# Optimization experiments

Measured on AMD Instinct MI355X. Metric: run time of the kernel, lower is better.

Reference implementation:

```python
import jax, jax.numpy as jnp
import numpy as np

B, S, D, H = 2, 2048, 1024, 16
DK = D // H
MAX_REL = 2047          # clip range for relative distances
REL_DIM = 64            # rel_embedding dim, summed over


def setup_inputs() -> dict:
    key = jax.random.key(0)
    ks = jax.random.split(key, 12)
    sc = 1.0 / np.sqrt(D)
    inp = {
        "q": jax.random.normal(ks[0], (B, S, D), jnp.float32),
        "k": jax.random.normal(ks[1], (B, S, D), jnp.float32),
        "v": jax.random.normal(ks[2], (B, S, D), jnp.float32),
        "Wq": jax.random.normal(ks[3], (D, D), jnp.float32) * sc,
        "bq": jnp.zeros((D,), jnp.float32),
        "Wk": jax.random.normal(ks[4], (D, D), jnp.float32) * sc,
        "bk": jnp.zeros((D,), jnp.float32),
        "Wv": jax.random.normal(ks[5], (D, D), jnp.float32) * sc,
        "bv": jnp.zeros((D,), jnp.float32),
        "Wo": jax.random.normal(ks[6], (D, D), jnp.float32) * sc,
        "bo": jnp.zeros((D,), jnp.float32),
        "rel_table": jax.random.normal(ks[7], (2 * MAX_REL + 1, REL_DIM), jnp.float32) * 0.02,
        "mask": jnp.tril(jnp.ones((1, 1, S, S), jnp.bool_)),  # causal
    }
    return inp


def reference(q, k, v, Wq, bq, Wk, bk, Wv, bv, Wo, bo, rel_table, mask):
    def split_heads(x):
        # [B,S,D] -> [B,H,S,DK]
        return x.reshape(B, -1, H, DK).transpose(0, 2, 1, 3)

    Q = split_heads(q @ Wq + bq)
    K = split_heads(k @ Wk + bk)
    V = split_heads(v @ Wv + bv)

    scores = jnp.einsum("bhqd,bhkd->bhqk", Q, K) / jnp.sqrt(jnp.float32(DK))

    # relative position bias: table[clip(j - i)] summed over rel dim -> [S,S]
    rel_idx = jnp.clip(jnp.arange(S)[None, :] - jnp.arange(S)[:, None],
                       -MAX_REL, MAX_REL) + MAX_REL
    rel_bias = rel_table[rel_idx].sum(-1)  # [S,S]
    scores = scores + rel_bias[None, None]

    scores = jnp.where(mask, scores, jnp.float32(-1e20))
    attn = jax.nn.softmax(scores, axis=-1)

    out = jnp.einsum("bhqk,bhkd->bhqd", attn, V)
    out = out.transpose(0, 2, 1, 3).reshape(B, -1, D)
    return out @ Wo + bo
```

## Files before the change

kernel.cpp:

```cpp
#include <hip/hip_runtime.h>

#define SEQ 2048
#define DIM 1024
#define NH 16
#define HD 64
#define NB 2

typedef __bf16 bf16x8 __attribute__((ext_vector_type(8)));
typedef float f32x4 __attribute__((ext_vector_type(4)));
typedef float f32x4v __attribute__((ext_vector_type(4)));
typedef float f32x4u __attribute__((ext_vector_type(4), aligned(4)));
typedef unsigned short us8 __attribute__((ext_vector_type(8)));
typedef unsigned short us4 __attribute__((ext_vector_type(4)));

#define LOG2E 1.44269504f

__device__ __forceinline__ unsigned short bfbits(float f) {
  __bf16 h = (__bf16)f;
  return __builtin_bit_cast(unsigned short, h);
}

__global__ __launch_bounds__(256) void wconv4_kernel(
    const float* __restrict__ W0, const float* __restrict__ W1,
    const float* __restrict__ W2, const float* __restrict__ W3,
    unsigned short* __restrict__ Wt, const float* __restrict__ rel_table,
    float* __restrict__ relsum, const float* __restrict__ Aq,
    const float* __restrict__ Ak, const float* __restrict__ Av,
    unsigned short* __restrict__ Bq, unsigned short* __restrict__ Bk,
    unsigned short* __restrict__ Bv) {
  int z = blockIdx.z;
  int tid = threadIdx.x;
  if (z == 4) {
    int ti = blockIdx.y * 16 + blockIdx.x;
    int i = ti * 256 + tid;
    if (i < 4095) {
      const f32x4v* row = reinterpret_cast<const f32x4v*>(rel_table + (size_t)i * 64);
      float s = 0.f;
      for (int d = 0; d < 16; ++d) {
        f32x4v v = row[d];
        s += v[0] + v[1] + v[2] + v[3];
      }
      relsum[i] = s * LOG2E;
    }
    return;
  }
  if (z >= 5) {
    const float* src = (z == 5) ? Aq : (z == 6) ? Ak : Av;
    unsigned short* dst = (z == 5) ? Bq : (z == 6) ? Bk : Bv;
    int bid2 = blockIdx.y * 16 + blockIdx.x;
    int c0 = bid2 * 256 + tid;
    for (int j = 0; j < 8; ++j) {
      size_t e = ((size_t)(c0 + j * 65536)) * 8;
      f32x4v v0 = *reinterpret_cast<const f32x4v*>(src + e);
      f32x4v v1 = *reinterpret_cast<const f32x4v*>(src + e + 4);
      us8 o;
      o[0] = bfbits(v0[0]); o[1] = bfbits(v0[1]); o[2] = bfbits(v0[2]); o[3] = bfbits(v0[3]);
      o[4] = bfbits(v1[0]); o[5] = bfbits(v1[1]); o[6] = bfbits(v1[2]); o[7] = bfbits(v1[3]);
      *reinterpret_cast<us8*>(dst + e) = o;
    }
    return;
  }
  __shared__ unsigned short T[64][68];
  const float* W = (z == 0) ? W0 : (z == 1) ? W1 : (z == 2) ? W2 : W3;
  unsigned short* out = Wt + (size_t)z * 1024 * 1024;
  int r0 = blockIdx.y * 64;
  int c0 = blockIdx.x * 64;
  for (int it = 0; it < 4; ++it) {
    int s = tid + it * 256;
    int r = s >> 4;
    int c4 = (s & 15) * 4;
    f32x4v v = *reinterpret_cast<const f32x4v*>(W + (size_t)(r0 + r) * 1024 + c0 + c4);
    us4 o;
    o[0] = bfbits(v[0]); o[1] = bfbits(v[1]); o[2] = bfbits(v[2]); o[3] = bfbits(v[3]);
    *reinterpret_cast<us4*>(&T[r][c4]) = o;
  }
  __syncthreads();
  for (int it = 0; it < 2; ++it) {
    int s = tid + it * 256;
    int n = s >> 3;
    int k8 = (s & 7) * 8;
    us8 o;
    for (int e = 0; e < 8; ++e) o[e] = T[k8 + e][n];
    *reinterpret_cast<us8*>(out + (size_t)(c0 + n) * 1024 + r0 + k8) = o;
  }
}

__global__ __launch_bounds__(256) void gemm_qkv_kernel(
    const unsigned short* __restrict__ Aq, const unsigned short* __restrict__ Ak,
    const unsigned short* __restrict__ Av, const unsigned short* __restrict__ WTb,
    const float* __restrict__ bq, const float* __restrict__ bk,
    const float* __restrict__ bv, unsigned short* __restrict__ Qb,
    unsigned short* __restrict__ Kb, unsigned short* __restrict__ Vt,
    float qscale) {
  constexpr int N = 1024, K = 1024;
  int o = (blockIdx.x & 7) * 192 + (blockIdx.x >> 3);
  int z = o >> 9;
  int r2 = o & 511;
  int row0 = (r2 >> 4) * 128;
  int col0 = (r2 & 15) * 64;
  const unsigned short* A = (z == 0) ? Aq : (z == 1) ? Ak : Av;
  const unsigned short* WT = WTb + (size_t)z * N * K;
  const float* bias = (z == 0) ? bq : (z == 1) ? bk : bv;
  float oscale = (z == 0) ? qscale : 1.0f;

  int tid = threadIdx.x;
  int w = tid >> 6;
  int lane = tid & 63;
  int lg = lane >> 4;
  int li = lane & 15;
  int wr = (w >> 1) * 64;
  int wc = (w & 1) * 32;

  __shared__ unsigned short As[2][128][72];
  __shared__ unsigned short Ws[2][64][72];

  us8 ab16[4];
  us8 wreg[2];

#define GLOAD(KS)                                                         \
  {                                                                       \
    int k0 = (KS) * 64;                                                   \
    for (int it = 0; it < 4; ++it) {                                      \
      int s = tid + it * 256;                                             \
      int r = s >> 3;                                                     \
      int cg = (s & 7) * 8;                                               \
      ab16[it] = *reinterpret_cast<const us8*>(                           \
          A + (size_t)(row0 + r) * K + k0 + cg);                          \
    }                                                                     \
    for (int it = 0; it < 2; ++it) {                                      \
      int s = tid + it * 256;                                             \
      int c = s >> 3;                                                     \
      int kg = (s & 7) * 8;                                               \
      wreg[it] = *reinterpret_cast<const us8*>(                           \
          WT + (size_t)(col0 + c) * K + k0 + kg);                         \
    }                                                                     \
  }

#define SWRITE(B)                                                         \
  {                                                                       \
    for (int it = 0; it < 4; ++it) {                                      \
      int s = tid + it * 256;                                             \
      int r = s >> 3;                                                     \
      int cg = (s & 7) * 8;                                               \
      *reinterpret_cast<us8*>(&As[B][r][cg]) = ab16[it];                  \
    }                                                                     \
    for (int it = 0; it < 2; ++it) {                                      \
      int s = tid + it * 256;                                             \
      int c = s >> 3;                                                     \
      int kg = (s & 7) * 8;                                               \
      *reinterpret_cast<us8*>(&Ws[B][c][kg]) = wreg[it];                  \
    }                                                                     \
  }

  f32x4 acc[4][2] = {};

  GLOAD(0);
  SWRITE(0);
  GLOAD(1);
  __syncthreads();

  for (int ks = 0; ks < 16; ++ks) {
    if (ks < 15) SWRITE((ks + 1) & 1);
    if (ks < 14) GLOAD(ks + 2);
    int B = ks & 1;
    for (int kk = 0; kk < 2; ++kk) {
      bf16x8 af[4], bfr[2];
      for (int m = 0; m < 4; ++m)
        af[m] = *reinterpret_cast<const bf16x8*>(&As[B][wr + m * 16 + li][kk * 32 + lg * 8]);
      for (int n = 0; n < 2; ++n)
        bfr[n] = *reinterpret_cast<const bf16x8*>(&Ws[B][wc + n * 16 + li][kk * 32 + lg * 8]);
      for (int m = 0; m < 4; ++m)
        for (int n = 0; n < 2; ++n)
          acc[m][n] = __builtin_amdgcn_mfma_f32_16x16x32_bf16(af[m], bfr[n], acc[m][n], 0, 0, 0);
    }
    __syncthreads();
  }

  for (int m = 0; m < 4; ++m)
    for (int n = 0; n < 2; ++n) {
      int row = row0 + wr + m * 16 + lg * 4;
      int col = col0 + wc + n * 16 + li;
      float v4[4];
      for (int r = 0; r < 4; ++r) v4[r] = (acc[m][n][r] + bias[col]) * oscale;
      if (z == 2) {
        int bb = row >> 11, seq = row & 2047;
        int hh = col >> 6, dk = col & 63;
        us4 o4;
        o4[0] = bfbits(v4[0]); o4[1] = bfbits(v4[1]);
        o4[2] = bfbits(v4[2]); o4[3] = bfbits(v4[3]);
        *reinterpret_cast<us4*>(
            Vt + ((size_t)(bb * NH + hh) * HD + dk) * SEQ + seq) = o4;
      } else {
        unsigned short* Cp = (z == 0) ? Qb : Kb;
        for (int r = 0; r < 4; ++r)
          Cp[(size_t)(row + r) * N + col] = bfbits(v4[r]);
      }
    }
#undef GLOAD
#undef SWRITE
}

__global__ __launch_bounds__(256) void gemm_out_kernel(
    const unsigned short* __restrict__ A, const unsigned short* __restrict__ WT,
    const float* __restrict__ bias, float* __restrict__ Cp) {
  constexpr int N = 1024, K = 1024;
  int o = ((blockIdx.x & 7) << 6) | (blockIdx.x >> 3);
  int col0 = (o & 15) * 64;
  int row0 = (o >> 4) * 128;
  int tid = threadIdx.x;
  int w = tid >> 6;
  int lane = tid & 63;
  int lg = lane >> 4;
  int li = lane & 15;
  int wr = (w >> 1) * 64;
  int wc = (w & 1) * 32;

  __shared__ unsigned short As[2][128][72];
  __shared__ unsigned short Ws[2][64][72];

  us8 ab16[4];
  us8 wreg[2];

#define GLOAD(KS)                                                         \
  {                                                                       \
    int k0 = (KS) * 64;                                                   \
    for (int it = 0; it < 4; ++it) {                                      \
      int s = tid + it * 256;                                             \
      int r = s >> 3;                                                     \
      int cg = (s & 7) * 8;                                               \
      ab16[it] = *reinterpret_cast<const us8*>(                           \
          A + (size_t)(row0 + r) * K + k0 + cg);                          \
    }                                                                     \
    for (int it = 0; it < 2; ++it) {                                      \
      int s = tid + it * 256;                                             \
      int c = s >> 3;                                                     \
      int kg = (s & 7) * 8;                                               \
      wreg[it] = *reinterpret_cast<const us8*>(                           \
          WT + (size_t)(col0 + c) * K + k0 + kg);                         \
    }                                                                     \
  }

#define SWRITE(B)                                                         \
  {                                                                       \
    for (int it = 0; it < 4; ++it) {                                      \
      int s = tid + it * 256;                                             \
      int r = s >> 3;                                                     \
      int cg = (s & 7) * 8;                                               \
      *reinterpret_cast<us8*>(&As[B][r][cg]) = ab16[it];                  \
    }                                                                     \
    for (int it = 0; it < 2; ++it) {                                      \
      int s = tid + it * 256;                                             \
      int c = s >> 3;                                                     \
      int kg = (s & 7) * 8;                                               \
      *reinterpret_cast<us8*>(&Ws[B][c][kg]) = wreg[it];                  \
    }                                                                     \
  }

  f32x4 acc[4][2] = {};

  GLOAD(0);
  SWRITE(0);
  GLOAD(1);
  __syncthreads();

  for (int ks = 0; ks < 16; ++ks) {
    if (ks < 15) SWRITE((ks + 1) & 1);
    if (ks < 14) GLOAD(ks + 2);
    int B = ks & 1;
    for (int kk = 0; kk < 2; ++kk) {
      bf16x8 af[4], bfr[2];
      for (int m = 0; m < 4; ++m)
        af[m] = *reinterpret_cast<const bf16x8*>(&As[B][wr + m * 16 + li][kk * 32 + lg * 8]);
      for (int n = 0; n < 2; ++n)
        bfr[n] = *reinterpret_cast<const bf16x8*>(&Ws[B][wc + n * 16 + li][kk * 32 + lg * 8]);
      for (int m = 0; m < 4; ++m)
        for (int n = 0; n < 2; ++n)
          acc[m][n] = __builtin_amdgcn_mfma_f32_16x16x32_bf16(af[m], bfr[n], acc[m][n], 0, 0, 0);
    }
    __syncthreads();
  }

  for (int m = 0; m < 4; ++m)
    for (int n = 0; n < 2; ++n)
      for (int r = 0; r < 4; ++r) {
        int row = row0 + wr + m * 16 + lg * 4 + r;
        int col = col0 + wc + n * 16 + li;
        Cp[(size_t)row * N + col] = acc[m][n][r] + bias[col];
      }
#undef GLOAD
#undef SWRITE
}

__global__ __launch_bounds__(256) void attn_kernel(
    const unsigned short* __restrict__ Qb, const unsigned short* __restrict__ Kb,
    const unsigned short* __restrict__ Vt, const float* __restrict__ relsum,
    unsigned short* __restrict__ Ob) {
  int o = ((blockIdx.x & 7) << 6) | (blockIdx.x >> 3);
  int p = o & 15;
  int h = (o >> 4) & 15;
  int b = o >> 8;

  int tid = threadIdx.x;
  int w = tid >> 6;
  int lane = tid & 63;
  int lg = lane >> 4;
  int li = lane & 15;

  __shared__ unsigned short Ks[128][72];
  __shared__ unsigned short VtF[2][64 * 72];
  __shared__ __bf16 Ps[4][16][136];
  __shared__ float rel_lds[2176];

  for (int it = 0; it < 3; ++it) {
    int slot = tid + it * 256;
    if (slot < 544)
      *reinterpret_cast<f32x4v*>(&rel_lds[slot * 4]) =
          *reinterpret_cast<const f32x4v*>(&relsum[slot * 4]);
  }

  int key0 = tid >> 3;
  int cg0 = (tid & 7) * 8;
  int dk0 = tid >> 3;
  int k8 = (tid & 7) * 8;
  const unsigned short* kptr = Kb + ((size_t)(b * SEQ + key0)) * DIM + h * HD + cg0;
  const unsigned short* vtp = Vt + ((size_t)(b * NH + h) * HD + dk0) * SEQ + k8;

  unsigned vidx0 = ((unsigned)(dk0 * 72 + k8)) ^ ((((unsigned)dk0 >> 3) & 7u) << 3);
  unsigned vidx1 = ((unsigned)((dk0 + 32) * 72 + k8)) ^
                   ((((unsigned)(dk0 + 32) >> 3) & 7u) << 3);

  us8 krg[4], vrg[4];

#define LOAD_REGS(TT)                                                     \
  {                                                                       \
    size_t koff = (size_t)(TT) * 128 * DIM;                               \
    krg[0] = *reinterpret_cast<const us8*>(kptr + koff);                  \
    krg[1] = *reinterpret_cast<const us8*>(kptr + koff + 32 * DIM);       \
    krg[2] = *reinterpret_cast<const us8*>(kptr + koff + 64 * DIM);       \
    krg[3] = *reinterpret_cast<const us8*>(kptr + koff + 96 * DIM);       \
    vrg[0] = *reinterpret_cast<const us8*>(vtp + (TT) * 128);             \
    vrg[1] = *reinterpret_cast<const us8*>(vtp + 32 * SEQ + (TT) * 128);  \
    vrg[2] = *reinterpret_cast<const us8*>(vtp + (TT) * 128 + 64);        \
    vrg[3] = *reinterpret_cast<const us8*>(vtp + 32 * SEQ + (TT) * 128 + 64); \
  }

#define WRITE_TILE()                                                     \
  {                                                                      \
    *reinterpret_cast<us8*>(&Ks[key0][cg0]) = krg[0];                    \
    *reinterpret_cast<us8*>(&Ks[key0 + 32][cg0]) = krg[1];               \
    *reinterpret_cast<us8*>(&Ks[key0 + 64][cg0]) = krg[2];               \
    *reinterpret_cast<us8*>(&Ks[key0 + 96][cg0]) = krg[3];               \
    *reinterpret_cast<us8*>(&VtF[0][vidx0]) = vrg[0];                    \
    *reinterpret_cast<us8*>(&VtF[0][vidx1]) = vrg[1];                    \
    *reinterpret_cast<us8*>(&VtF[1][vidx0]) = vrg[2];                    \
    *reinterpret_cast<us8*>(&VtF[1][vidx1]) = vrg[3];                    \
  }

  LOAD_REGS(0);

  for (int ph = 0; ph < 2; ++ph) {
    int qt = ph ? p : (31 - p);
    int nkv = (qt + 2) >> 1;

    int qrow = qt * 64 + w * 16 + li;
    const unsigned short* qb = Qb + ((size_t)(b * SEQ + qrow)) * DIM + h * HD;
    bf16x8 qa0 = *reinterpret_cast<const bf16x8*>(qb + lg * 8);
    bf16x8 qa1 = *reinterpret_cast<const bf16x8*>(qb + 32 + lg * 8);

    f32x4 o_acc[4] = {};
    float m_row[4], l_row[4];
    for (int r = 0; r < 4; ++r) { m_row[r] = -3e38f; l_row[r] = 0.f; }
    int i0 = qt * 64 + w * 16 + lg * 4;

    for (int t = 0; t < nkv; ++t) {
      __syncthreads();
      WRITE_TILE();
      __syncthreads();

      if (!(ph == 1 && t == nkv - 1)) {
        int nextT = (t + 1 < nkv) ? (t + 1) : 0;
        LOAD_REGS(nextT);
      }

      f32x4 s_acc[8] = {};
      __builtin_amdgcn_s_setprio(1);
      for (int kk = 0; kk < 2; ++kk) {
        bf16x8 qa = kk ? qa1 : qa0;
        for (int n = 0; n < 8; ++n) {
          bf16x8 kb = *reinterpret_cast<const bf16x8*>(&Ks[n * 16 + li][kk * 32 + lg * 8]);
          s_acc[n] = __builtin_amdgcn_mfma_f32_16x16x32_bf16(qa, kb, s_acc[n], 0, 0, 0);
        }
      }
      __builtin_amdgcn_s_setprio(0);

      float tmax[4] = {-3e38f, -3e38f, -3e38f, -3e38f};
      int Cbase = t * 128 - (qt * 64 + w * 16 + lg * 4) + li + 2047;
      if (t == nkv - 1) {
        for (int n = 0; n < 8; ++n) {
          int Cn = Cbase + n * 16;
          f32x4u rel4 = *reinterpret_cast<const f32x4u*>(&rel_lds[Cn - 3]);
          for (int r = 0; r < 4; ++r) {
            float sv = s_acc[n][r] + rel4[3 - r];
            sv = (Cn - r > 2047) ? -1e30f : sv;
            s_acc[n][r] = sv;
            tmax[r] = fmaxf(tmax[r], sv);
          }
        }
      } else {
        for (int n = 0; n < 8; ++n) {
          int Cn = Cbase + n * 16;
          f32x4u rel4 = *reinterpret_cast<const f32x4u*>(&rel_lds[Cn - 3]);
          for (int r = 0; r < 4; ++r) {
            float sv = s_acc[n][r] + rel4[3 - r];
            s_acc[n][r] = sv;
            tmax[r] = fmaxf(tmax[r], sv);
          }
        }
      }

      bool okl = true;
      for (int r = 0; r < 4; ++r) okl &= (tmax[r] <= m_row[r] + 8.f);
      if (!__all(okl)) {
        for (int msk = 1; msk < 16; msk <<= 1)
          for (int r = 0; r < 4; ++r)
            tmax[r] = fmaxf(tmax[r], __shfl_xor(tmax[r], msk));
        for (int r = 0; r < 4; ++r) {
          float mn = fmaxf(m_row[r], tmax[r]);
          float al = exp2f(m_row[r] - mn);
          m_row[r] = mn;
          l_row[r] *= al;
          o_acc[0][r] *= al; o_acc[1][r] *= al;
          o_acc[2][r] *= al; o_acc[3][r] *= al;
        }
      }

      for (int n = 0; n < 8; ++n)
        for (int r = 0; r < 4; ++r) {
          float e = exp2f(s_acc[n][r] - m_row[r]);
          s_acc[n][r] = e;
          l_row[r] += e;
        }

      for (int n = 0; n < 8; ++n)
        for (int r = 0; r < 4; ++r)
          Ps[w][lg * 4 + r][n * 16 + li] = (__bf16)s_acc[n][r];
      asm volatile("s_waitcnt lgkmcnt(0)" ::: "memory");
      __builtin_amdgcn_sched_barrier(0);

      __builtin_amdgcn_s_setprio(1);
      for (int kstep = 0; kstep < 4; ++kstep) {
        int half = kstep >> 1;
        int kk = kstep & 1;
        bf16x8 pa = *reinterpret_cast<const bf16x8*>(&Ps[w][li][kstep * 32 + lg * 8]);
        for (int n = 0; n < 4; ++n) {
          int dk = n * 16 + li;
          unsigned idx = ((unsigned)(dk * 72 + kk * 32 + lg * 8)) ^
                         ((((unsigned)dk >> 3) & 7u) << 3);
          bf16x8 vb = *reinterpret_cast<const bf16x8*>(&VtF[half][idx]);
          o_acc[n] = __builtin_amdgcn_mfma_f32_16x16x32_bf16(pa, vb, o_acc[n], 0, 0, 0);
        }
      }
      __builtin_amdgcn_s_setprio(0);
    }

    for (int msk = 1; msk < 16; msk <<= 1)
      for (int r = 0; r < 4; ++r) l_row[r] += __shfl_xor(l_row[r], msk);
    float inv_l[4];
    for (int r = 0; r < 4; ++r) inv_l[r] = 1.f / l_row[r];
    for (int n = 0; n < 4; ++n)
      for (int r = 0; r < 4; ++r) {
        int row = i0 + r;
        int dk = n * 16 + li;
        Ob[((size_t)(b * SEQ + row)) * DIM + h * HD + dk] =
            bfbits(o_acc[n][r] * inv_l[r]);
      }
  }
#undef LOAD_REGS
#undef WRITE_TILE
}

extern "C" void kernel_launch(void* const* d_in, const int* in_sizes, int n_in,
                              void* d_out, int out_size, void* d_ws, size_t ws_size,
                              hipStream_t stream) {
  const float* q = (const float*)d_in[0];
  const float* k = (const float*)d_in[1];
  const float* v = (const float*)d_in[2];
  const float* Wq = (const float*)d_in[3];
  const float* bq = (const float*)d_in[4];
  const float* Wk = (const float*)d_in[5];
  const float* bk = (const float*)d_in[6];
  const float* Wv = (const float*)d_in[7];
  const float* bv = (const float*)d_in[8];
  const float* Wo = (const float*)d_in[9];
  const float* bo = (const float*)d_in[10];
  const float* rel = (const float*)d_in[11];

  char* ws = (char*)d_ws;
  const size_t MATB = (size_t)NB * SEQ * DIM * sizeof(unsigned short);
  const size_t WTE = (size_t)DIM * DIM;
  unsigned short* Qb = (unsigned short*)(ws);
  unsigned short* Kb = (unsigned short*)(ws + MATB);
  unsigned short* Vt = (unsigned short*)(ws + 2 * MATB);
  unsigned short* Ob = (unsigned short*)(ws + 3 * MATB);
  float* relsum = (float*)(ws + 4 * MATB);
  unsigned short* WT = (unsigned short*)(ws + 4 * MATB + 65536);

  unsigned short* Abq = (unsigned short*)d_out;
  unsigned short* Abk = (unsigned short*)d_out + (size_t)NB * SEQ * DIM;
  unsigned short* Abv = Ob;

  wconv4_kernel<<<dim3(16, 16, 8), 256, 0, stream>>>(
      Wq, Wk, Wv, Wo, WT, rel, relsum, q, k, v, Abq, Abk, Abv);

  const float qscale = 0.125f * LOG2E;
  gemm_qkv_kernel<<<dim3(1536), 256, 0, stream>>>(Abq, Abk, Abv, WT, bq, bk, bv,
                                                  Qb, Kb, Vt, qscale);

  attn_kernel<<<dim3(512), 256, 0, stream>>>(Qb, Kb, Vt, relsum, Ob);

  gemm_out_kernel<<<dim3(512), 256, 0, stream>>>(Ob, WT + 3 * WTE, bo, (float*)d_out);
}
```

Baseline: 136.9 us.

## Split paired causal query tiles into one block each with 64-key tiles

The attention kernel no longer pairs a long and a short query tile in one block for load balance. It now launches one block per (batch, head, query tile), 1024 blocks in total, ordered longest-first and grouped by XCD. KV tiles shrink from 128 to 64 keys, so the causal diagonal tile wastes less masked work and LDS and register use drop, which may allow higher occupancy. In exchange each block does less work per barrier, K/V loads are repeated across more blocks, and load balance relies on the hardware scheduler rather than explicit pairing.

```diff
diff --git a/kernel.cpp b/kernel.cpp
--- a/kernel.cpp
+++ b/kernel.cpp
@@ -295,10 +295,12 @@
     const unsigned short* __restrict__ Qb, const unsigned short* __restrict__ Kb,
     const unsigned short* __restrict__ Vt, const float* __restrict__ relsum,
     unsigned short* __restrict__ Ob) {
-  int o = ((blockIdx.x & 7) << 6) | (blockIdx.x >> 3);
-  int p = o & 15;
-  int h = (o >> 4) & 15;
-  int b = o >> 8;
+  int r0_ = blockIdx.x >> 3;
+  int xcd = blockIdx.x & 7;
+  int qt = 31 - (r0_ >> 2);
+  int bh = xcd * 4 + (r0_ & 3);
+  int h = bh & 15;
+  int b = bh >> 4;
 
   int tid = threadIdx.x;
   int w = tid >> 6;
@@ -306,14 +308,14 @@
   int lg = lane >> 4;
   int li = lane & 15;
 
-  __shared__ unsigned short Ks[128][72];
-  __shared__ unsigned short VtF[2][64 * 72];
-  __shared__ __bf16 Ps[4][16][136];
-  __shared__ float rel_lds[2176];
+  __shared__ unsigned short Ks[64][72];
+  __shared__ unsigned short VtF[64 * 72];
+  __shared__ __bf16 Ps[4][16][72];
+  __shared__ float rel_lds[2112];
 
   for (int it = 0; it < 3; ++it) {
     int slot = tid + it * 256;
-    if (slot < 544)
+    if (slot < 528)
       *reinterpret_cast<f32x4v*>(&rel_lds[slot * 4]) =
           *reinterpret_cast<const f32x4v*>(&relsum[slot * 4]);
   }
@@ -329,152 +331,134 @@
   unsigned vidx1 = ((unsigned)((dk0 + 32) * 72 + k8)) ^
                    ((((unsigned)(dk0 + 32) >> 3) & 7u) << 3);
 
-  us8 krg[4], vrg[4];
+  us8 krg0, krg1, vrg0, vrg1;
 
 #define LOAD_REGS(TT)                                                     \
   {                                                                       \
-    size_t koff = (size_t)(TT) * 128 * DIM;                               \
-    krg[0] = *reinterpret_cast<const us8*>(kptr + koff);                  \
-    krg[1] = *reinterpret_cast<const us8*>(kptr + koff + 32 * DIM);       \
-    krg[2] = *reinterpret_cast<const us8*>(kptr + koff + 64 * DIM);       \
-    krg[3] = *reinterpret_cast<const us8*>(kptr + koff + 96 * DIM);       \
-    vrg[0] = *reinterpret_cast<const us8*>(vtp + (TT) * 128);             \
-    vrg[1] = *reinterpret_cast<const us8*>(vtp + 32 * SEQ + (TT) * 128);  \
-    vrg[2] = *reinterpret_cast<const us8*>(vtp + (TT) * 128 + 64);        \
-    vrg[3] = *reinterpret_cast<const us8*>(vtp + 32 * SEQ + (TT) * 128 + 64); \
-  }
-
-#define WRITE_TILE()                                                     \
-  {                                                                      \
-    *reinterpret_cast<us8*>(&Ks[key0][cg0]) = krg[0];                    \
-    *reinterpret_cast<us8*>(&Ks[key0 + 32][cg0]) = krg[1];               \
-    *reinterpret_cast<us8*>(&Ks[key0 + 64][cg0]) = krg[2];               \
-    *reinterpret_cast<us8*>(&Ks[key0 + 96][cg0]) = krg[3];               \
-    *reinterpret_cast<us8*>(&VtF[0][vidx0]) = vrg[0];                    \
-    *reinterpret_cast<us8*>(&VtF[0][vidx1]) = vrg[1];                    \
-    *reinterpret_cast<us8*>(&VtF[1][vidx0]) = vrg[2];                    \
-    *reinterpret_cast<us8*>(&VtF[1][vidx1]) = vrg[3];                    \
+    size_t koff = (size_t)(TT) * 64 * DIM;                                \
+    krg0 = *reinterpret_cast<const us8*>(kptr + koff);                    \
+    krg1 = *reinterpret_cast<const us8*>(kptr + koff + 32 * DIM);         \
+    vrg0 = *reinterpret_cast<const us8*>(vtp + (TT) * 64);                \
+    vrg1 = *reinterpret_cast<const us8*>(vtp + 32 * SEQ + (TT) * 64);     \
+  }
+
+#define WRITE_TILE()                                                      \
+  {                                                                       \
+    *reinterpret_cast<us8*>(&Ks[key0][cg0]) = krg0;                       \
+    *reinterpret_cast<us8*>(&Ks[key0 + 32][cg0]) = krg1;                  \
+    *reinterpret_cast<us8*>(&VtF[vidx0]) = vrg0;                          \
+    *reinterpret_cast<us8*>(&VtF[vidx1]) = vrg1;                          \
   }
 
   LOAD_REGS(0);
 
-  for (int ph = 0; ph < 2; ++ph) {
-    int qt = ph ? p : (31 - p);
-    int nkv = (qt + 2) >> 1;
-
-    int qrow = qt * 64 + w * 16 + li;
-    const unsigned short* qb = Qb + ((size_t)(b * SEQ + qrow)) * DIM + h * HD;
-    bf16x8 qa0 = *reinterpret_cast<const bf16x8*>(qb + lg * 8);
-    bf16x8 qa1 = *reinterpret_cast<const bf16x8*>(qb + 32 + lg * 8);
-
-    f32x4 o_acc[4] = {};
-    float m_row[4], l_row[4];
-    for (int r = 0; r < 4; ++r) { m_row[r] = -3e38f; l_row[r] = 0.f; }
-    int i0 = qt * 64 + w * 16 + lg * 4;
-
-    for (int t = 0; t < nkv; ++t) {
-      __syncthreads();
-      WRITE_TILE();
-      __syncthreads();
-
-      if (!(ph == 1 && t == nkv - 1)) {
-        int nextT = (t + 1 < nkv) ? (t + 1) : 0;
-        LOAD_REGS(nextT);
-      }
-
-      f32x4 s_acc[8] = {};
-      __builtin_amdgcn_s_setprio(1);
-      for (int kk = 0; kk < 2; ++kk) {
-        bf16x8 qa = kk ? qa1 : qa0;
-        for (int n = 0; n < 8; ++n) {
-          bf16x8 kb = *reinterpret_cast<const bf16x8*>(&Ks[n * 16 + li][kk * 32 + lg * 8]);
-          s_acc[n] = __builtin_amdgcn_mfma_f32_16x16x32_bf16(qa, kb, s_acc[n], 0, 0, 0);
+  int qrow = qt * 64 + w * 16 + li;
+  const unsigned short* qb = Qb + ((size_t)(b * SEQ + qrow)) * DIM + h * HD;
+  bf16x8 qa0 = *reinterpret_cast<const bf16x8*>(qb + lg * 8);
+  bf16x8 qa1 = *reinterpret_cast<const bf16x8*>(qb + 32 + lg * 8);
+
+  f32x4 o_acc[4] = {};
+  float m_row[4], l_row[4];
+  for (int r = 0; r < 4; ++r) { m_row[r] = -3e38f; l_row[r] = 0.f; }
+  int i0 = qt * 64 + w * 16 + lg * 4;
+
+  for (int t = 0; t <= qt; ++t) {
+    __syncthreads();
+    WRITE_TILE();
+    __syncthreads();
+
+    if (t < qt) LOAD_REGS(t + 1);
+
+    f32x4 s_acc[4] = {};
+    __builtin_amdgcn_s_setprio(1);
+    for (int kk = 0; kk < 2; ++kk) {
+      bf16x8 qa = kk ? qa1 : qa0;
+      for (int n = 0; n < 4; ++n) {
+        bf16x8 kb = *reinterpret_cast<const bf16x8*>(&Ks[n * 16 + li][kk * 32 + lg * 8]);
+        s_acc[n] = __builtin_amdgcn_mfma_f32_16x16x32_bf16(qa, kb, s_acc[n], 0, 0, 0);
+      }
+    }
+    __builtin_amdgcn_s_setprio(0);
+
+    float tmax[4] = {-3e38f, -3e38f, -3e38f, -3e38f};
+    int Cbase = (t - qt) * 64 - (w * 16 + lg * 4) + li + 2047;
+    if (t == qt) {
+      for (int n = 0; n < 4; ++n) {
+        int Cn = Cbase + n * 16;
+        f32x4u rel4 = *reinterpret_cast<const f32x4u*>(&rel_lds[Cn - 3]);
+        for (int r = 0; r < 4; ++r) {
+          float sv = s_acc[n][r] + rel4[3 - r];
+          sv = (Cn - r > 2047) ? -1e30f : sv;
+          s_acc[n][r] = sv;
+          tmax[r] = fmaxf(tmax[r], sv);
         }
       }
-      __builtin_amdgcn_s_setprio(0);
-
-      float tmax[4] = {-3e38f, -3e38f, -3e38f, -3e38f};
-      int Cbase = t * 128 - (qt * 64 + w * 16 + lg * 4) + li + 2047;
-      if (t == nkv - 1) {
-        for (int n = 0; n < 8; ++n) {
-          int Cn = Cbase + n * 16;
-          f32x4u rel4 = *reinterpret_cast<const f32x4u*>(&rel_lds[Cn - 3]);
-          for (int r = 0; r < 4; ++r) {
-            float sv = s_acc[n][r] + rel4[3 - r];
-            sv = (Cn - r > 2047) ? -1e30f : sv;
-            s_acc[n][r] = sv;
-            tmax[r] = fmaxf(tmax[r], sv);
-          }
+    } else {
+      for (int n = 0; n < 4; ++n) {
+        int Cn = Cbase + n * 16;
+        f32x4u rel4 = *reinterpret_cast<const f32x4u*>(&rel_lds[Cn - 3]);
+        for (int r = 0; r < 4; ++r) {
+          float sv = s_acc[n][r] + rel4[3 - r];
+          s_acc[n][r] = sv;
+          tmax[r] = fmaxf(tmax[r], sv);
         }
-      } else {
-        for (int n = 0; n < 8; ++n) {
-          int Cn = Cbase + n * 16;
-          f32x4u rel4 = *reinterpret_cast<const f32x4u*>(&rel_lds[Cn - 3]);
-          for (int r = 0; r < 4; ++r) {
-            float sv = s_acc[n][r] + rel4[3 - r];
-            s_acc[n][r] = sv;
-            tmax[r] = fmaxf(tmax[r], sv);
-          }
-        }
-      }
-
-      bool okl = true;
-      for (int r = 0; r < 4; ++r) okl &= (tmax[r] <= m_row[r] + 8.f);
-      if (!__all(okl)) {
-        for (int msk = 1; msk < 16; msk <<= 1)
-          for (int r = 0; r < 4; ++r)
-            tmax[r] = fmaxf(tmax[r], __shfl_xor(tmax[r], msk));
-        for (int r = 0; r < 4; ++r) {
-          float mn = fmaxf(m_row[r], tmax[r]);
-          float al = exp2f(m_row[r] - mn);
-          m_row[r] = mn;
-          l_row[r] *= al;
-          o_acc[0][r] *= al; o_acc[1][r] *= al;
-          o_acc[2][r] *= al; o_acc[3][r] *= al;
-        }
-      }
-
-      for (int n = 0; n < 8; ++n)
-        for (int r = 0; r < 4; ++r) {
-          float e = exp2f(s_acc[n][r] - m_row[r]);
-          s_acc[n][r] = e;
-          l_row[r] += e;
-        }
-
-      for (int n = 0; n < 8; ++n)
+      }
+    }
+
+    bool okl = true;
+    for (int r = 0; r < 4; ++r) okl &= (tmax[r] <= m_row[r] + 8.f);
+    if (!__all(okl)) {
+      for (int msk = 1; msk < 16; msk <<= 1)
         for (int r = 0; r < 4; ++r)
-          Ps[w][lg * 4 + r][n * 16 + li] = (__bf16)s_acc[n][r];
-      asm volatile("s_waitcnt lgkmcnt(0)" ::: "memory");
-      __builtin_amdgcn_sched_barrier(0);
-
-      __builtin_amdgcn_s_setprio(1);
-      for (int kstep = 0; kstep < 4; ++kstep) {
-        int half = kstep >> 1;
-        int kk = kstep & 1;
-        bf16x8 pa = *reinterpret_cast<const bf16x8*>(&Ps[w][li][kstep * 32 + lg * 8]);
-        for (int n = 0; n < 4; ++n) {
-          int dk = n * 16 + li;
-          unsigned idx = ((unsigned)(dk * 72 + kk * 32 + lg * 8)) ^
-                         ((((unsigned)dk >> 3) & 7u) << 3);
-          bf16x8 vb = *reinterpret_cast<const bf16x8*>(&VtF[half][idx]);
-          o_acc[n] = __builtin_amdgcn_mfma_f32_16x16x32_bf16(pa, vb, o_acc[n], 0, 0, 0);
-        }
-      }
-      __builtin_amdgcn_s_setprio(0);
-    }
-
-    for (int msk = 1; msk < 16; msk <<= 1)
-      for (int r = 0; r < 4; ++r) l_row[r] += __shfl_xor(l_row[r], msk);
-    float inv_l[4];
-    for (int r = 0; r < 4; ++r) inv_l[r] = 1.f / l_row[r];
+          tmax[r] = fmaxf(tmax[r], __shfl_xor(tmax[r], msk));
+      for (int r = 0; r < 4; ++r) {
+        float mn = fmaxf(m_row[r], tmax[r]);
+        float al = exp2f(m_row[r] - mn);
+        m_row[r] = mn;
+        l_row[r] *= al;
+        o_acc[0][r] *= al; o_acc[1][r] *= al;
+        o_acc[2][r] *= al; o_acc[3][r] *= al;
+      }
+    }
+
     for (int n = 0; n < 4; ++n)
       for (int r = 0; r < 4; ++r) {
-        int row = i0 + r;
+        float e = exp2f(s_acc[n][r] - m_row[r]);
+        s_acc[n][r] = e;
+        l_row[r] += e;
+      }
+
+    for (int n = 0; n < 4; ++n)
+      for (int r = 0; r < 4; ++r)
+        Ps[w][lg * 4 + r][n * 16 + li] = (__bf16)s_acc[n][r];
+    asm volatile("s_waitcnt lgkmcnt(0)" ::: "memory");
+    __builtin_amdgcn_sched_barrier(0);
+
+    __builtin_amdgcn_s_setprio(1);
+    for (int kk = 0; kk < 2; ++kk) {
+      bf16x8 pa = *reinterpret_cast<const bf16x8*>(&Ps[w][li][kk * 32 + lg * 8]);
+      for (int n = 0; n < 4; ++n) {
         int dk = n * 16 + li;
-        Ob[((size_t)(b * SEQ + row)) * DIM + h * HD + dk] =
-            bfbits(o_acc[n][r] * inv_l[r]);
-      }
-  }
+        unsigned idx = ((unsigned)(dk * 72 + kk * 32 + lg * 8)) ^
+                       ((((unsigned)dk >> 3) & 7u) << 3);
+        bf16x8 vb = *reinterpret_cast<const bf16x8*>(&VtF[idx]);
+        o_acc[n] = __builtin_amdgcn_mfma_f32_16x16x32_bf16(pa, vb, o_acc[n], 0, 0, 0);
+      }
+    }
+    __builtin_amdgcn_s_setprio(0);
+  }
+
+  for (int msk = 1; msk < 16; msk <<= 1)
+    for (int r = 0; r < 4; ++r) l_row[r] += __shfl_xor(l_row[r], msk);
+  float inv_l[4];
+  for (int r = 0; r < 4; ++r) inv_l[r] = 1.f / l_row[r];
+  for (int n = 0; n < 4; ++n)
+    for (int r = 0; r < 4; ++r) {
+      int row = i0 + r;
+      int dk = n * 16 + li;
+      Ob[((size_t)(b * SEQ + row)) * DIM + h * HD + dk] =
+          bfbits(o_acc[n][r] * inv_l[r]);
+    }
 #undef LOAD_REGS
 #undef WRITE_TILE
 }
@@ -516,7 +500,7 @@
   gemm_qkv_kernel<<<dim3(1536), 256, 0, stream>>>(Abq, Abk, Abv, WT, bq, bk, bv,
                                                   Qb, Kb, Vt, qscale);
 
-  attn_kernel<<<dim3(512), 256, 0, stream>>>(Qb, Kb, Vt, relsum, Ob);
+  attn_kernel<<<dim3(1024), 256, 0, stream>>>(Qb, Kb, Vt, relsum, Ob);
 
   gemm_out_kernel<<<dim3(512), 256, 0, stream>>>(Ob, WT + 3 * WTE, bo, (float*)d_out);
 }
```

Measured after the change: 130.7 us. 4.6% less time.
